# Kernel optimization log

Measured on AMD Instinct MI355X. Metric: run time of the kernel, lower is better.

The kernel has to match this reference:

```python
import jax, jax.numpy as jnp
import numpy as np

TAU = 2.0
V_TH = 1.0
SG_ALPHA = 4.0  # spikingjelly surrogate.Sigmoid default

@jax.custom_vjp
def spike_fn(u):
    # heaviside(u) with sigmoid surrogate gradient; u = v - v_threshold
    return (u >= 0.0).astype(u.dtype)

def _spike_fwd(u):
    return spike_fn(u), u

def _spike_bwd(u, g):
    s = jax.nn.sigmoid(SG_ALPHA * u)
    return (g * SG_ALPHA * s * (1.0 - s),)

spike_fn.defvjp(_spike_fwd, _spike_bwd)

def lif_scan(h):
    # h: [T, B, D] input currents; multi-step LIF with hard reset to 0,
    # decay_input=True: v = v + (h - v) / tau
    def step(v, h_t):
        v = v + (h_t - v) / TAU
        s = spike_fn(v - V_TH)
        v = v * (1.0 - jax.lax.stop_gradient(s))  # detach_reset=True, v_reset=0
        return v, s
    v0 = jnp.zeros_like(h[0])
    _, spikes = jax.lax.scan(step, v0, h)
    return spikes  # [T, B, D]

def setup_inputs() -> dict:
    key = jax.random.key(0)
    k_x, k_w1, k_b1, k_w2, k_b2 = jax.random.split(key, 5)
    T, B, D, C = 32, 512, 1024, 1000
    lim1 = 1.0 / np.sqrt(D)
    return {
        "x": jax.random.normal(k_x, (T, B, D), dtype=jnp.float32),
        "W1": jax.random.uniform(k_w1, (D, D), jnp.float32, -lim1, lim1),
        "b1": jax.random.uniform(k_b1, (D,), jnp.float32, -lim1, lim1),
        "W2": jax.random.uniform(k_w2, (C, D), jnp.float32, -lim1, lim1),
        "b2": jax.random.uniform(k_b2, (C,), jnp.float32, -lim1, lim1),
    }

def reference(x, W1, b1, W2, b2):
    # linear_1: [T,B,D] @ [D,D]^T + b1
    h = jnp.einsum('tbd,ed->tbe', x, W1) + b1
    s = lif_scan(h)                               # [T,B,D] spikes in {0,1}
    y = jnp.einsum('tbd,cd->tbc', s, W2) + b2     # [T,B,C]
    y = y.mean(axis=0)                            # [B,C]
    return jax.nn.log_softmax(y, axis=1)
```

## Files before the change

kernel.cpp:

```cpp
#include <hip/hip_runtime.h>
#include <math.h>

#define T_STEPS 32
#define B_SZ    512
#define D_SZ    1024
#define C_SZ    1000
#define KZ      8
#define HP      132

typedef __bf16 bf16x8 __attribute__((ext_vector_type(8)));
typedef float  f32x4  __attribute__((ext_vector_type(4)));

__device__ __forceinline__ unsigned short f2bf(float f) {
    unsigned u = __float_as_uint(f);
    unsigned r = u + 0x7FFFu + ((u >> 16) & 1u);
    return (unsigned short)(r >> 16);
}
__device__ __forceinline__ float bf2f(unsigned short b) {
    return __uint_as_float(((unsigned)b) << 16);
}

__device__ __forceinline__ void async_copy16(const void* g, void* l) {
    __builtin_amdgcn_global_load_lds(
        (const __attribute__((address_space(1))) unsigned int*)g,
        (__attribute__((address_space(3))) unsigned int*)l,
        16, 0, 0);
}

__device__ __forceinline__ bf16x8 cvt8(const float4 u, const float4 v) {
    bf16x8 r;
    r[0] = (__bf16)u.x; r[1] = (__bf16)u.y; r[2] = (__bf16)u.z; r[3] = (__bf16)u.w;
    r[4] = (__bf16)v.x; r[5] = (__bf16)v.y; r[6] = (__bf16)v.z; r[7] = (__bf16)v.w;
    return r;
}

#define NX4   4194304
#define NW14  262144
#define NW24  256000
#define NWTOT (NW14 + NW24)
#define NCTOT (NX4 + NW14 + NW24)

__global__ __launch_bounds__(256) void cast_all_k(
    const float* __restrict__ X,  unsigned short* __restrict__ X_bf,
    const float* __restrict__ W1, unsigned short* __restrict__ W1_bf,
    const float* __restrict__ W2, unsigned short* __restrict__ W2_bf)
{
    const int idx = blockIdx.x * 256 + threadIdx.x;
    const float4* s; ushort4* d; int j;
    if (idx < NX4)              { s = (const float4*)X;  d = (ushort4*)X_bf;  j = idx; }
    else if (idx < NX4 + NW14)  { s = (const float4*)W1; d = (ushort4*)W1_bf; j = idx - NX4; }
    else                        { s = (const float4*)W2; d = (ushort4*)W2_bf; j = idx - NX4 - NW14; }
    const float4 v = s[j];
    ushort4 o;
    o.x = f2bf(v.x); o.y = f2bf(v.y); o.z = f2bf(v.z); o.w = f2bf(v.w);
    d[j] = o;
}

__global__ __launch_bounds__(256) void cast_w_k(
    const float* __restrict__ W1, unsigned short* __restrict__ W1_bf,
    const float* __restrict__ W2, unsigned short* __restrict__ W2_bf)
{
    const int idx = blockIdx.x * 256 + threadIdx.x;
    const float4* s; ushort4* d; int j;
    if (idx < NW14) { s = (const float4*)W1; d = (ushort4*)W1_bf; j = idx; }
    else            { s = (const float4*)W2; d = (ushort4*)W2_bf; j = idx - NW14; }
    const float4 v = s[j];
    ushort4 o;
    o.x = f2bf(v.x); o.y = f2bf(v.y); o.z = f2bf(v.z); o.w = f2bf(v.w);
    d[j] = o;
}

__global__ __launch_bounds__(512, 2) void gemm1_scan256_k(
    const unsigned short* __restrict__ Xb, const unsigned short* __restrict__ Bm,
    const float* __restrict__ bias, unsigned short* __restrict__ cnt)
{
    __shared__ __align__(16) unsigned short smem[65536];

    const int tid  = threadIdx.x;
    const int wave = tid >> 6;
    const int lane = tid & 63;
    const int lm   = lane & 15;
    const int quad = lane >> 4;
    const int wm   = (wave >> 2) * 128;
    const int wn   = (wave & 3) * 64;

    const int wgid = (blockIdx.x & 7) * 32 + (blockIdx.x >> 3);
    const int yb = wgid >> 2;
    const int xb = wgid & 3;
    const int b0 = yb * 8;
    const int n0 = xb * 256;

    f32x4 acc[8][4];
    #pragma unroll
    for (int i = 0; i < 8; ++i)
        #pragma unroll
        for (int j = 0; j < 4; ++j)
            acc[i][j] = (f32x4){0.f, 0.f, 0.f, 0.f};

    size_t aoff[4], boff[4];
    unsigned ldsoffp[4];
    #pragma unroll
    for (int p = 0; p < 4; ++p) {
        const int s   = p * 512 + tid;
        const int rho = s >> 3;
        const int gq  = (s & 7) ^ (rho & 7);
        aoff[p] = (size_t)((rho >> 3) * 512 + b0 + (rho & 7)) * D_SZ + gq * 8;
        boff[p] = (size_t)(n0 + rho) * D_SZ + gq * 8;
        ldsoffp[p] = (unsigned)(p * 512 + wave * 64) * 16u;
    }
    const int fq0 = quad ^ (lm & 7);

#define STG_A(cb_, k0_) do {                                                     \
        char* ab_ = (char*)smem + (cb_) * 32768;                                 \
        _Pragma("unroll")                                                        \
        for (int p = 0; p < 4; ++p)                                              \
            async_copy16(Xb + aoff[p] + (k0_), ab_ + ldsoffp[p]);                \
    } while (0)

#define STG_B(cb_, k0_) do {                                                     \
        char* bb_ = (char*)smem + 65536 + (cb_) * 32768;                         \
        _Pragma("unroll")                                                        \
        for (int p = 0; p < 4; ++p)                                              \
            async_copy16(Bm + boff[p] + (k0_), bb_ + ldsoffp[p]);                \
    } while (0)

#define READ_A(mi0_) do {                                                        \
        _Pragma("unroll")                                                        \
        for (int m2 = 0; m2 < 2; ++m2) {                                         \
            const int rw_ = wm + ((mi0_) + m2) * 16 + lm;                        \
            af[m2][0] = Ar[rw_ * 8 + fq0];                                       \
            af[m2][1] = Ar[rw_ * 8 + (fq0 ^ 4)];                                 \
        }                                                                        \
    } while (0)

#define MFMA2(mi0_) do {                                                         \
        __builtin_amdgcn_s_setprio(1);                                           \
        _Pragma("unroll")                                                        \
        for (int kk = 0; kk < 2; ++kk)                                           \
            _Pragma("unroll")                                                    \
            for (int m2 = 0; m2 < 2; ++m2)                                       \
                _Pragma("unroll")                                                \
                for (int ni = 0; ni < 4; ++ni)                                   \
                    acc[(mi0_) + m2][ni] = __builtin_amdgcn_mfma_f32_16x16x32_bf16( \
                        af[m2][kk], bfr[ni][kk], acc[(mi0_) + m2][ni], 0, 0, 0); \
        __builtin_amdgcn_s_setprio(0);                                           \
    } while (0)

    STG_A(0, 0);
    STG_B(0, 0);
    __syncthreads();

    #pragma unroll 2
    for (int t = 0; t < 16; ++t) {
        const int c  = t & 1;
        const bf16x8* Ar = (const bf16x8*)((const char*)smem + c * 32768);
        const bf16x8* Br = (const bf16x8*)((const char*)smem + 65536 + c * 32768);
        const int kn = (t + 1) * 64;
        bf16x8 bfr[4][2], af[2][2];

        #pragma unroll
        for (int ni = 0; ni < 4; ++ni) {
            const int rw = (wn + ni * 16 + lm) * 8;
            bfr[ni][0] = Br[rw + fq0];
            bfr[ni][1] = Br[rw + (fq0 ^ 4)];
        }
        READ_A(0);
        if (t < 15) STG_A(c ^ 1, kn);
        __builtin_amdgcn_s_barrier();
        MFMA2(0);
        __builtin_amdgcn_s_barrier();

        READ_A(2);
        if (t < 15) STG_B(c ^ 1, kn);
        __builtin_amdgcn_s_barrier();
        MFMA2(2);
        __builtin_amdgcn_s_barrier();

        READ_A(4);
        __builtin_amdgcn_s_barrier();
        MFMA2(4);
        __builtin_amdgcn_s_barrier();

        READ_A(6);
        __builtin_amdgcn_s_barrier();
        MFMA2(6);
        __syncthreads();
    }

#undef STG_A
#undef STG_B
#undef READ_A
#undef MFMA2

    #pragma unroll
    for (int ni = 0; ni < 4; ++ni) {
        const int col = wn + ni * 16 + lm;
        const float bv = bias[n0 + col];
        #pragma unroll
        for (int mi = 0; mi < 8; ++mi) {
            const f32x4 v = acc[mi][ni];
            #pragma unroll
            for (int q = 0; q < 4; ++q) {
                const int row = wm + mi * 16 + quad * 4 + q;
                smem[row * 256 + (col ^ (((row >> 2) & 3) << 4))] = f2bf(v[q] + bv);
            }
        }
    }
    __syncthreads();

    {
        const unsigned* smemU = (const unsigned*)smem;
        const int uc = tid & 127;
        const int h4 = tid >> 7;
        #pragma unroll
        for (int g = 0; g < 2; ++g) {
            const int bb = h4 + g * 4;
            float v0 = 0.f, cv0 = 0.f, v1 = 0.f, cv1 = 0.f;
            #pragma unroll
            for (int t2 = 0; t2 < T_STEPS; ++t2) {
                const int rho = t2 * 8 + bb;
                const unsigned u =
                    smemU[rho * 128 + (uc ^ (((rho >> 2) & 3) << 3))];
                const float h0 = bf2f((unsigned short)(u & 0xFFFFu));
                const float h1 = bf2f((unsigned short)(u >> 16));
                v0 = 0.5f * (v0 + h0);
                const float s0 = (v0 >= 1.0f) ? 1.0f : 0.0f;
                cv0 += s0; v0 *= (1.0f - s0);
                v1 = 0.5f * (v1 + h1);
                const float s1 = (v1 >= 1.0f) ? 1.0f : 0.0f;
                cv1 += s1; v1 *= (1.0f - s1);
            }
            ushort2 o;
            o.x = f2bf(cv0); o.y = f2bf(cv1);
            *(ushort2*)&cnt[(size_t)(b0 + bb) * D_SZ + n0 + 2 * uc] = o;
        }
    }
}

__global__ __launch_bounds__(256) void gemm1_scan_f32_k(
    const float* __restrict__ X, const unsigned short* __restrict__ Bm,
    const float* __restrict__ bias, unsigned short* __restrict__ cnt)
{
    __shared__ __align__(16) unsigned short smem[32768];

    const int tid  = threadIdx.x;
    const int wave = tid >> 6;
    const int lane = tid & 63;
    const int lm   = lane & 15;
    const int quad = lane >> 4;
    const int wm   = (wave >> 1) * 64;
    const int wn   = (wave & 1) * 64;

    const int f  = blockIdx.x;
    const int rr = f >> 9;
    const int cc = f & 7;
    const int ss = (f >> 3) & 63;
    const int xb = ss & 7;
    const int yb = rr * 64 + (ss >> 3) * 8 + cc;
    const int b0 = yb * 4;
    const int n0 = xb * 128;

    f32x4 acc[4][4];
    #pragma unroll
    for (int i = 0; i < 4; ++i)
        #pragma unroll
        for (int j = 0; j < 4; ++j)
            acc[i][j] = (f32x4){0.f, 0.f, 0.f, 0.f};

    int srow[4], sgq[4];
    size_t arowoff[4];
    unsigned ldsoffB[4];
    #pragma unroll
    for (int p = 0; p < 4; ++p) {
        const int s = p * 256 + tid;
        const int rho = s >> 3;
        srow[p] = rho;
        sgq[p]  = (s & 7) ^ (rho & 7);
        arowoff[p] = (size_t)((rho >> 2) * 512 + b0 + (rho & 3)) * D_SZ;
        ldsoffB[p] = (unsigned)(p * 256 + wave * 64) * 16u;
    }
    const int fq0 = quad ^ (lm & 7);

    float4 au[4], av[4];

#define LOAD_A(k0_) do {                                                        \
        _Pragma("unroll")                                                       \
        for (int p = 0; p < 4; ++p) {                                           \
            const float* srcp = X + arowoff[p] + (k0_) + sgq[p] * 8;            \
            au[p] = *(const float4*)(srcp);                                     \
            av[p] = *(const float4*)(srcp + 4);                                 \
        }                                                                       \
    } while (0)

#define STAGE_B(buf_, k0_) do {                                                 \
        char* bdst = (char*)(smem + 16384 + (buf_) * 8192);                     \
        _Pragma("unroll")                                                       \
        for (int p = 0; p < 4; ++p)                                             \
            async_copy16(Bm + (size_t)(n0 + srow[p]) * D_SZ + (k0_) + sgq[p] * 8,\
                         bdst + ldsoffB[p]);                                    \
    } while (0)

#define WRITE_A(buf_) do {                                                      \
        bf16x8* adst = (bf16x8*)(smem + (buf_) * 8192);                         \
        _Pragma("unroll")                                                       \
        for (int p = 0; p < 4; ++p)                                             \
            adst[p * 256 + tid] = cvt8(au[p], av[p]);                           \
    } while (0)

#define COMPUTE(buf_) do {                                                      \
        const bf16x8* Ar = (const bf16x8*)(smem + (buf_) * 8192);               \
        const bf16x8* Br = (const bf16x8*)(smem + 16384 + (buf_) * 8192);       \
        __builtin_amdgcn_s_setprio(1);                                          \
        _Pragma("unroll")                                                       \
        for (int kk = 0; kk < 2; ++kk) {                                        \
            const int fqk = fq0 ^ (kk * 4);                                     \
            bf16x8 af[4], bfr[4];                                               \
            _Pragma("unroll")                                                   \
            for (int i2 = 0; i2 < 4; ++i2) {                                    \
                af[i2]  = Ar[(wm + i2 * 16 + lm) * 8 + fqk];                    \
                bfr[i2] = Br[(wn + i2 * 16 + lm) * 8 + fqk];                    \
            }                                                                   \
            _Pragma("unroll")                                                   \
            for (int mi = 0; mi < 4; ++mi)                                      \
                _Pragma("unroll")                                               \
                for (int ni = 0; ni < 4; ++ni)                                  \
                    acc[mi][ni] = __builtin_amdgcn_mfma_f32_16x16x32_bf16(      \
                        af[mi], bfr[ni], acc[mi][ni], 0, 0, 0);                 \
        }                                                                       \
        __builtin_amdgcn_s_setprio(0);                                          \
    } while (0)

    LOAD_A(0);
    STAGE_B(0, 0);
    WRITE_A(0);
    __syncthreads();
    LOAD_A(64);
    STAGE_B(1, 64);

    for (int i = 0; i < 14; i += 2) {
        COMPUTE(0);
        WRITE_A(1);
        __syncthreads();
        LOAD_A((i + 2) * 64);
        STAGE_B(0, (i + 2) * 64);

        COMPUTE(1);
        WRITE_A(0);
        __syncthreads();
        LOAD_A((i + 3) * 64);
        STAGE_B(1, (i + 3) * 64);
    }
    COMPUTE(0);
    WRITE_A(1);
    __syncthreads();
    COMPUTE(1);
    __syncthreads();

#undef LOAD_A
#undef STAGE_B
#undef WRITE_A
#undef COMPUTE

    #pragma unroll
    for (int ni = 0; ni < 4; ++ni) {
        const int nn = wn + ni * 16 + lm;
        const float bv = bias[n0 + nn];
        #pragma unroll
        for (int mi = 0; mi < 4; ++mi) {
            const f32x4 v = acc[mi][ni];
            #pragma unroll
            for (int q = 0; q < 4; ++q)
                smem[(wm + mi * 16 + quad * 4 + q) * HP + nn] = f2bf(v[q] + bv);
        }
    }
    __syncthreads();

    {
        const unsigned* smemU = (const unsigned*)smem;
        const int bb = tid >> 6;
        const int c2 = tid & 63;
        float v0 = 0.f, cv0 = 0.f, v1 = 0.f, cv1 = 0.f;
        #pragma unroll
        for (int t = 0; t < T_STEPS; ++t) {
            const unsigned u = smemU[(t * 4 + bb) * (HP / 2) + c2];
            const float h0 = bf2f((unsigned short)(u & 0xFFFFu));
            const float h1 = bf2f((unsigned short)(u >> 16));
            v0 = 0.5f * (v0 + h0);
            const float s0 = (v0 >= 1.0f) ? 1.0f : 0.0f;
            cv0 += s0; v0 *= (1.0f - s0);
            v1 = 0.5f * (v1 + h1);
            const float s1 = (v1 >= 1.0f) ? 1.0f : 0.0f;
            cv1 += s1; v1 *= (1.0f - s1);
        }
        ushort2 o;
        o.x = f2bf(cv0); o.y = f2bf(cv1);
        *(ushort2*)&cnt[(size_t)(b0 + bb) * D_SZ + n0 + 2 * c2] = o;
    }
}

__global__ __launch_bounds__(256) void gemm2_splitk_k(
    const unsigned short* __restrict__ A, const unsigned short* __restrict__ Bm,
    float* __restrict__ partial)
{
    __shared__ __align__(16) unsigned short As[128 * 32];
    __shared__ __align__(16) unsigned short Bs[128 * 32];

    const int tid  = threadIdx.x;
    const int wave = tid >> 6;
    const int lane = tid & 63;
    const int lm   = lane & 15;
    const int quad = lane >> 4;
    const int wm   = (wave >> 1) * 64;
    const int wn   = (wave & 1) * 64;
    const int n0   = blockIdx.x * 128;
    const int m0   = blockIdx.y * 128;
    const int kz   = blockIdx.z;

    f32x4 acc[4][4];
    #pragma unroll
    for (int i = 0; i < 4; ++i)
        #pragma unroll
        for (int j = 0; j < 4; ++j)
            acc[i][j] = (f32x4){0.f, 0.f, 0.f, 0.f};

    int srow[2], sgq[2];
    unsigned ldsoff[2];
    #pragma unroll
    for (int p = 0; p < 2; ++p) {
        const int s = p * 256 + tid;
        srow[p] = s >> 2;
        sgq[p]  = (s & 3) ^ ((srow[p] >> 1) & 3);
        ldsoff[p] = (unsigned)(p * 256 + wave * 64) * 16u;
    }
    const int fq = quad ^ ((lm >> 1) & 3);

    const int kbeg = kz * (D_SZ / KZ);
    for (int k0 = kbeg; k0 < kbeg + D_SZ / KZ; k0 += 32) {
        #pragma unroll
        for (int p = 0; p < 2; ++p) {
            async_copy16(A + (size_t)(m0 + srow[p]) * D_SZ + k0 + sgq[p] * 8,
                         (char*)As + ldsoff[p]);
            int brow = n0 + srow[p];
            if (brow > C_SZ - 1) brow = C_SZ - 1;
            async_copy16(Bm + (size_t)brow * D_SZ + k0 + sgq[p] * 8,
                         (char*)Bs + ldsoff[p]);
        }
        __syncthreads();

        bf16x8 af[4], bfr[4];
        #pragma unroll
        for (int i = 0; i < 4; ++i) {
            af[i]  = ((const bf16x8*)As)[(wm + i * 16 + lm) * 4 + fq];
            bfr[i] = ((const bf16x8*)Bs)[(wn + i * 16 + lm) * 4 + fq];
        }
        #pragma unroll
        for (int mi = 0; mi < 4; ++mi)
            #pragma unroll
            for (int ni = 0; ni < 4; ++ni)
                acc[mi][ni] = __builtin_amdgcn_mfma_f32_16x16x32_bf16(
                    af[mi], bfr[ni], acc[mi][ni], 0, 0, 0);
        __syncthreads();
    }

    #pragma unroll
    for (int ni = 0; ni < 4; ++ni) {
        const int nn = n0 + wn + ni * 16 + lm;
        if (nn >= C_SZ) continue;
        #pragma unroll
        for (int mi = 0; mi < 4; ++mi) {
            const f32x4 v = acc[mi][ni];
            #pragma unroll
            for (int q = 0; q < 4; ++q) {
                const int mm = m0 + wm + mi * 16 + quad * 4 + q;
                partial[((size_t)kz * B_SZ + mm) * C_SZ + nn] = v[q];
            }
        }
    }
}

__global__ __launch_bounds__(256) void reduce_lsm_k(
    const float* __restrict__ partial, const float* __restrict__ b2,
    float* __restrict__ out)
{
    __shared__ float red_max[4];
    __shared__ float red_sum[4];

    const int b   = blockIdx.x;
    const int tid = threadIdx.x;

    float vals[4];
    float m = -1e30f;
    #pragma unroll
    for (int k = 0; k < 4; ++k) {
        const int c = tid + k * 256;
        if (c < C_SZ) {
            float s = 0.f;
            #pragma unroll
            for (int z = 0; z < KZ; ++z)
                s += partial[((size_t)z * B_SZ + b) * C_SZ + c];
            vals[k] = s * (1.0f / (float)T_STEPS) + b2[c];
        } else {
            vals[k] = -1e30f;
        }
        m = fmaxf(m, vals[k]);
    }
    #pragma unroll
    for (int off = 32; off > 0; off >>= 1)
        m = fmaxf(m, __shfl_down(m, off, 64));
    const int wave = tid >> 6;
    const int lane = tid & 63;
    if (lane == 0) red_max[wave] = m;
    __syncthreads();
    m = fmaxf(fmaxf(red_max[0], red_max[1]), fmaxf(red_max[2], red_max[3]));

    float s = 0.f;
    #pragma unroll
    for (int k = 0; k < 4; ++k) {
        const int c = tid + k * 256;
        if (c < C_SZ) s += __expf(vals[k] - m);
    }
    #pragma unroll
    for (int off = 32; off > 0; off >>= 1)
        s += __shfl_down(s, off, 64);
    if (lane == 0) red_sum[wave] = s;
    __syncthreads();
    s = red_sum[0] + red_sum[1] + red_sum[2] + red_sum[3];

    const float lse = m + logf(s);
    #pragma unroll
    for (int k = 0; k < 4; ++k) {
        const int c = tid + k * 256;
        if (c < C_SZ) out[(size_t)b * C_SZ + c] = vals[k] - lse;
    }
}

extern "C" void kernel_launch(void* const* d_in, const int* in_sizes, int n_in,
                              void* d_out, int out_size, void* d_ws, size_t ws_size,
                              hipStream_t stream)
{
    const float* x  = (const float*)d_in[0];
    const float* W1 = (const float*)d_in[1];
    const float* b1 = (const float*)d_in[2];
    const float* W2 = (const float*)d_in[3];
    const float* b2 = (const float*)d_in[4];
    float* out = (float*)d_out;

    char* ws = (char*)d_ws;

    if (ws_size >= 38748160u) {
        unsigned short* X_bf    = (unsigned short*)(ws);
        float*          partial = (float*)(ws);
        unsigned short* W1_bf   = (unsigned short*)(ws + 33554432);
        unsigned short* W2_bf   = (unsigned short*)(ws + 35651584);
        unsigned short* cnt_bf  = (unsigned short*)(ws + 37699584);

        cast_all_k<<<NCTOT / 256, 256, 0, stream>>>(x, X_bf, W1, W1_bf, W2, W2_bf);
        gemm1_scan256_k<<<256, 512, 0, stream>>>(X_bf, W1_bf, b1, cnt_bf);
        {
            dim3 grid((C_SZ + 127) / 128, B_SZ / 128, KZ);
            gemm2_splitk_k<<<grid, 256, 0, stream>>>(cnt_bf, W2_bf, partial);
        }
        reduce_lsm_k<<<B_SZ, 256, 0, stream>>>(partial, b2, out);
    } else {
        unsigned short* W1_bf   = (unsigned short*)(ws);
        unsigned short* W2_bf   = (unsigned short*)(ws + 2097152);
        unsigned short* cnt_bf  = (unsigned short*)(ws + 4145152);
        float*          partial = (float*)(ws + 5193728);

        cast_w_k<<<NWTOT / 256, 256, 0, stream>>>(W1, W1_bf, W2, W2_bf);
        gemm1_scan_f32_k<<<(B_SZ / 4) * (D_SZ / 128), 256, 0, stream>>>(
            x, W1_bf, b1, cnt_bf);
        {
            dim3 grid((C_SZ + 127) / 128, B_SZ / 128, KZ);
            gemm2_splitk_k<<<grid, 256, 0, stream>>>(cnt_bf, W2_bf, partial);
        }
        reduce_lsm_k<<<B_SZ, 256, 0, stream>>>(partial, b2, out);
    }
}
```

Baseline: 152.2 us.

## Fuse split-K GEMM2 and log-softmax reduction into one kernel with grid barrier

Merges the split-K second GEMM and the partial-sum reduction plus log-softmax into a single persistent-style launch of 512 blocks. The first 256 blocks compute the split-K partials, all blocks meet at a software grid barrier built on atomics, and then each block reduces one batch row. This is meant to remove one kernel launch and the gap between launches. In exchange it adds a memset, spin-wait overhead, and relies on all 512 blocks being co-resident, which could deadlock or time out (the guard breaks the wait) if they are not.

```diff
diff --git a/kernel.cpp b/kernel.cpp
--- a/kernel.cpp
+++ b/kernel.cpp
@@ -7,6 +7,7 @@
 #define C_SZ    1000
 #define KZ      8
 #define HP      132
+#define RBLK    512
 
 typedef __bf16 bf16x8 __attribute__((ext_vector_type(8)));
 typedef float  f32x4  __attribute__((ext_vector_type(4)));
@@ -32,6 +33,26 @@
     r[0] = (__bf16)u.x; r[1] = (__bf16)u.y; r[2] = (__bf16)u.z; r[3] = (__bf16)u.w;
     r[4] = (__bf16)v.x; r[5] = (__bf16)v.y; r[6] = (__bf16)v.z; r[7] = (__bf16)v.w;
     return r;
+}
+
+__device__ __forceinline__ void grid_sync(unsigned* c, unsigned* e) {
+    __syncthreads();
+    if (threadIdx.x == 0) {
+        __threadfence();
+        atomicAdd(c, 1u);
+        int guard = 0;
+        while (__hip_atomic_load(c, __ATOMIC_RELAXED, __HIP_MEMORY_SCOPE_AGENT)
+               < (unsigned)RBLK) {
+            __builtin_amdgcn_s_sleep(8);
+            if (++guard > 4000000) break;
+        }
+        __threadfence();
+        if (atomicAdd(e, 1u) == (unsigned)RBLK - 1u) {
+            __hip_atomic_store(c, 0u, __ATOMIC_RELAXED, __HIP_MEMORY_SCOPE_AGENT);
+            __hip_atomic_store(e, 0u, __ATOMIC_RELAXED, __HIP_MEMORY_SCOPE_AGENT);
+        }
+    }
+    __syncthreads();
 }
 
 #define NX4   4194304
@@ -398,6 +419,145 @@
     }
 }
 
+__global__ __launch_bounds__(256, 2) void gemm2_reduce_k(
+    const unsigned short* __restrict__ A, const unsigned short* __restrict__ Bm,
+    const float* __restrict__ b2, float* __restrict__ partial,
+    float* __restrict__ out, unsigned* __restrict__ bar)
+{
+    __shared__ __align__(16) unsigned short smem[8192];
+
+    const int tid = threadIdx.x;
+    const int bid = blockIdx.x;
+
+    if (bid < 256) {
+        unsigned short* As = smem;
+        unsigned short* Bs = smem + 4096;
+
+        const int wave = tid >> 6;
+        const int lane = tid & 63;
+        const int lm   = lane & 15;
+        const int quad = lane >> 4;
+        const int wm   = (wave >> 1) * 64;
+        const int wn   = (wave & 1) * 64;
+        const int n0   = (bid & 7) * 128;
+        const int m0   = ((bid >> 3) & 3) * 128;
+        const int kz   = bid >> 5;
+
+        f32x4 acc[4][4];
+        #pragma unroll
+        for (int i = 0; i < 4; ++i)
+            #pragma unroll
+            for (int j = 0; j < 4; ++j)
+                acc[i][j] = (f32x4){0.f, 0.f, 0.f, 0.f};
+
+        int srow[2], sgq[2];
+        unsigned ldsoff[2];
+        #pragma unroll
+        for (int p = 0; p < 2; ++p) {
+            const int s = p * 256 + tid;
+            srow[p] = s >> 2;
+            sgq[p]  = (s & 3) ^ ((srow[p] >> 1) & 3);
+            ldsoff[p] = (unsigned)(p * 256 + wave * 64) * 16u;
+        }
+        const int fq = quad ^ ((lm >> 1) & 3);
+
+        const int kbeg = kz * (D_SZ / KZ);
+        for (int k0 = kbeg; k0 < kbeg + D_SZ / KZ; k0 += 32) {
+            #pragma unroll
+            for (int p = 0; p < 2; ++p) {
+                async_copy16(A + (size_t)(m0 + srow[p]) * D_SZ + k0 + sgq[p] * 8,
+                             (char*)As + ldsoff[p]);
+                int brow = n0 + srow[p];
+                if (brow > C_SZ - 1) brow = C_SZ - 1;
+                async_copy16(Bm + (size_t)brow * D_SZ + k0 + sgq[p] * 8,
+                             (char*)Bs + ldsoff[p]);
+            }
+            __syncthreads();
+
+            bf16x8 af[4], bfr[4];
+            #pragma unroll
+            for (int i = 0; i < 4; ++i) {
+                af[i]  = ((const bf16x8*)As)[(wm + i * 16 + lm) * 4 + fq];
+                bfr[i] = ((const bf16x8*)Bs)[(wn + i * 16 + lm) * 4 + fq];
+            }
+            #pragma unroll
+            for (int mi = 0; mi < 4; ++mi)
+                #pragma unroll
+                for (int ni = 0; ni < 4; ++ni)
+                    acc[mi][ni] = __builtin_amdgcn_mfma_f32_16x16x32_bf16(
+                        af[mi], bfr[ni], acc[mi][ni], 0, 0, 0);
+            __syncthreads();
+        }
+
+        #pragma unroll
+        for (int ni = 0; ni < 4; ++ni) {
+            const int nn = n0 + wn + ni * 16 + lm;
+            if (nn >= C_SZ) continue;
+            #pragma unroll
+            for (int mi = 0; mi < 4; ++mi) {
+                const f32x4 v = acc[mi][ni];
+                #pragma unroll
+                for (int q = 0; q < 4; ++q) {
+                    const int mm = m0 + wm + mi * 16 + quad * 4 + q;
+                    partial[((size_t)kz * B_SZ + mm) * C_SZ + nn] = v[q];
+                }
+            }
+        }
+    }
+    grid_sync(bar + 0, bar + 1);
+
+    {
+        float* red_max = (float*)smem;
+        float* red_sum = (float*)smem + 4;
+        const int b = bid;
+
+        float vals[4];
+        float m = -1e30f;
+        #pragma unroll
+        for (int k = 0; k < 4; ++k) {
+            const int c = tid + k * 256;
+            if (c < C_SZ) {
+                float s = 0.f;
+                #pragma unroll
+                for (int z = 0; z < KZ; ++z)
+                    s += partial[((size_t)z * B_SZ + b) * C_SZ + c];
+                vals[k] = s * (1.0f / (float)T_STEPS) + b2[c];
+            } else {
+                vals[k] = -1e30f;
+            }
+            m = fmaxf(m, vals[k]);
+        }
+        #pragma unroll
+        for (int off = 32; off > 0; off >>= 1)
+            m = fmaxf(m, __shfl_down(m, off, 64));
+        const int wave = tid >> 6;
+        const int lane = tid & 63;
+        if (lane == 0) red_max[wave] = m;
+        __syncthreads();
+        m = fmaxf(fmaxf(red_max[0], red_max[1]), fmaxf(red_max[2], red_max[3]));
+
+        float s = 0.f;
+        #pragma unroll
+        for (int k = 0; k < 4; ++k) {
+            const int c = tid + k * 256;
+            if (c < C_SZ) s += __expf(vals[k] - m);
+        }
+        #pragma unroll
+        for (int off = 32; off > 0; off >>= 1)
+            s += __shfl_down(s, off, 64);
+        if (lane == 0) red_sum[wave] = s;
+        __syncthreads();
+        s = red_sum[0] + red_sum[1] + red_sum[2] + red_sum[3];
+
+        const float lse = m + logf(s);
+        #pragma unroll
+        for (int k = 0; k < 4; ++k) {
+            const int c = tid + k * 256;
+            if (c < C_SZ) out[(size_t)b * C_SZ + c] = vals[k] - lse;
+        }
+    }
+}
+
 __global__ __launch_bounds__(256) void gemm2_splitk_k(
     const unsigned short* __restrict__ A, const unsigned short* __restrict__ Bm,
     float* __restrict__ partial)
@@ -547,20 +707,19 @@
 
     char* ws = (char*)d_ws;
 
-    if (ws_size >= 38748160u) {
+    if (ws_size >= 38748224u) {
         unsigned short* X_bf    = (unsigned short*)(ws);
         float*          partial = (float*)(ws);
         unsigned short* W1_bf   = (unsigned short*)(ws + 33554432);
         unsigned short* W2_bf   = (unsigned short*)(ws + 35651584);
         unsigned short* cnt_bf  = (unsigned short*)(ws + 37699584);
-
+        unsigned*       bar     = (unsigned*)(ws + 38748160);
+
+        (void)hipMemsetAsync(bar, 0, 16, stream);
         cast_all_k<<<NCTOT / 256, 256, 0, stream>>>(x, X_bf, W1, W1_bf, W2, W2_bf);
         gemm1_scan256_k<<<256, 512, 0, stream>>>(X_bf, W1_bf, b1, cnt_bf);
-        {
-            dim3 grid((C_SZ + 127) / 128, B_SZ / 128, KZ);
-            gemm2_splitk_k<<<grid, 256, 0, stream>>>(cnt_bf, W2_bf, partial);
-        }
-        reduce_lsm_k<<<B_SZ, 256, 0, stream>>>(partial, b2, out);
+        gemm2_reduce_k<<<RBLK, 256, 0, stream>>>(
+            cnt_bf, W2_bf, b2, partial, out, bar);
     } else {
         unsigned short* W1_bf   = (unsigned short*)(ws);
         unsigned short* W2_bf   = (unsigned short*)(ws + 2097152);
@@ -570,10 +729,8 @@
         cast_w_k<<<NWTOT / 256, 256, 0, stream>>>(W1, W1_bf, W2, W2_bf);
         gemm1_scan_f32_k<<<(B_SZ / 4) * (D_SZ / 128), 256, 0, stream>>>(
             x, W1_bf, b1, cnt_bf);
-        {
-            dim3 grid((C_SZ + 127) / 128, B_SZ / 128, KZ);
-            gemm2_splitk_k<<<grid, 256, 0, stream>>>(cnt_bf, W2_bf, partial);
-        }
+        dim3 g2((C_SZ + 127) / 128, B_SZ / 128, KZ);
+        gemm2_splitk_k<<<g2, 256, 0, stream>>>(cnt_bf, W2_bf, partial);
         reduce_lsm_k<<<B_SZ, 256, 0, stream>>>(partial, b2, out);
     }
 }
```

Measured after the change: 200.7 us. 1.32x slower.
